# Kernel tuning notes

Measured on AMD Instinct MI355X. Metric: run time of the kernel, lower is better.

The kernel has to match this reference:

```python
import jax, jax.numpy as jnp
import numpy as np

N_NODES = 50000


def gcn_conv(x, edge_index, W, b, n_nodes):
    # Linear transform first (as in PyG GCNConv), then normalized aggregation
    xw = x @ W  # [N, out]
    src, dst = edge_index[0], edge_index[1]
    loops = jnp.arange(n_nodes, dtype=src.dtype)
    s = jnp.concatenate([src, loops])  # add self-loops
    d = jnp.concatenate([dst, loops])
    deg = jax.ops.segment_sum(jnp.ones_like(s, dtype=xw.dtype), d, num_segments=n_nodes)
    dinv = jnp.where(deg > 0, jax.lax.rsqrt(deg), 0.0)
    norm = dinv[s] * dinv[d]  # [E+N]
    msg = xw[s] * norm[:, None]  # gather + scale
    out = jax.ops.segment_sum(msg, d, num_segments=n_nodes)  # scatter-add
    return out + b


def setup_inputs() -> dict:
    key = jax.random.key(0)
    k1, k2, k3, k4 = jax.random.split(key, 4)
    in_dim, hidden = 128, 128
    n_edges = 625000
    x = jax.random.normal(k1, (N_NODES, in_dim), dtype=jnp.float32)
    edge_index = jax.random.randint(k2, (2, n_edges), 0, N_NODES, dtype=jnp.int64)
    # glorot-ish scale
    W1 = jax.random.normal(k3, (in_dim, hidden), dtype=jnp.float32) * (1.0 / np.sqrt(in_dim))
    b1 = jnp.zeros((hidden,), dtype=jnp.float32)
    W2 = jax.random.normal(k4, (hidden, hidden), dtype=jnp.float32) * (1.0 / np.sqrt(hidden))
    b2 = jnp.zeros((hidden,), dtype=jnp.float32)
    return {"x": x, "edge_index": edge_index, "W1": W1, "b1": b1, "W2": W2, "b2": b2}


def reference(x, edge_index, W1, b1, W2, b2):
    n = x.shape[0]
    h = gcn_conv(x, edge_index, W1, b1, n)
    h = jax.nn.relu(h)
    # dropout(p=0.3) is identity in eval mode
    h = gcn_conv(h, edge_index, W2, b2, n)
    return jax.nn.relu(h)
```

## Files before the change

kernel.cpp:

```cpp
#include <hip/hip_runtime.h>
#include <hip/hip_bf16.h>

#define NNODES 50000
#define BKT 64
#define LP 136
#define NC 25
#define CCAP 40960
#define P0EPT 16
#define FINE 128
#define AGG_BLOCKS 2048

typedef short bf16x8 __attribute__((ext_vector_type(8)));
typedef float f32x4 __attribute__((ext_vector_type(4)));

__device__ __forceinline__ unsigned short f2bf_rn(float f) {
    unsigned int u = __float_as_uint(f);
    return (unsigned short)((u + 0x7fffu + ((u >> 16) & 1u)) >> 16);
}
__device__ __forceinline__ float bf_lo(unsigned int u) { return __uint_as_float(u << 16); }
__device__ __forceinline__ float bf_hi(unsigned int u) { return __uint_as_float(u & 0xffff0000u); }


__global__ __launch_bounds__(256) void k_wt(const float* __restrict__ W1,
                                            const float* __restrict__ W2,
                                            unsigned short* __restrict__ WT1,
                                            unsigned short* __restrict__ WT2,
                                            int* __restrict__ gcnt) {
    __shared__ float tile[128 * 129];
    int b = blockIdx.x, t = threadIdx.x;
    if (b == 0 && t < NC) gcnt[t] = 0;
    const float* W = b ? W2 : W1;
    unsigned short* WT = b ? WT2 : WT1;
    for (int idx = t; idx < 128 * 128; idx += 256)
        tile[(idx >> 7) * 129 + (idx & 127)] = W[idx];
    __syncthreads();
    for (int idx = t; idx < 128 * 128; idx += 256) {
        int c = idx >> 7, k = idx & 127;
        WT[c * 128 + k] = f2bf_rn(tile[k * 129 + c]);
    }
}


__global__ __launch_bounds__(256) void k_part(const int* __restrict__ src,
                                              const int* __restrict__ dst,
                                              int* __restrict__ gcnt,
                                              unsigned int* __restrict__ rec, int E) {
    __shared__ int lhist[NC];
    __shared__ int lbase[NC];
    int t = threadIdx.x;
    if (t < NC) lhist[t] = 0;
    __syncthreads();

    int e0 = (blockIdx.x * 256 + t) * P0EPT;
    unsigned int r[P0EPT];
    int cc[P0EPT];
    int lofs[P0EPT];
    int nv = 0;
    if (e0 + P0EPT <= E) {
#pragma unroll
        for (int k4 = 0; k4 < P0EPT / 4; ++k4) {
            int4 s4 = *(const int4*)&src[e0 + k4 * 4];
            int4 d4 = *(const int4*)&dst[e0 + k4 * 4];
            int ss[4] = {s4.x, s4.y, s4.z, s4.w};
            int dd[4] = {d4.x, d4.y, d4.z, d4.w};
#pragma unroll
            for (int k = 0; k < 4; ++k) {
                r[k4 * 4 + k] = (unsigned)(ss[k] & 0xffff) | ((unsigned)dd[k] << 16);
                cc[k4 * 4 + k] = dd[k] >> 11;
            }
        }
        nv = P0EPT;
    } else {
#pragma unroll
        for (int k = 0; k < P0EPT; ++k) {
            int e = e0 + k;
            if (e < E) {
                int s = src[e], d = dst[e];
                r[k] = (unsigned)(s & 0xffff) | ((unsigned)d << 16);
                cc[k] = d >> 11;
                nv = k + 1;
            } else {
                cc[k] = 0;
            }
        }
    }
#pragma unroll
    for (int k = 0; k < P0EPT; ++k)
        if (k < nv) lofs[k] = atomicAdd(&lhist[cc[k]], 1);
    __syncthreads();
    if (t < NC) lbase[t] = atomicAdd(&gcnt[t], lhist[t]);
    __syncthreads();
#pragma unroll
    for (int k = 0; k < P0EPT; ++k)
        if (k < nv) {
            int pos = lbase[cc[k]] + lofs[k];
            if (pos < CCAP) rec[(size_t)cc[k] * CCAP + pos] = r[k];
        }
}


__global__ __launch_bounds__(256) void k_bucket2(const unsigned int* __restrict__ rec,
                                                 const int* __restrict__ gcnt,
                                                 int* __restrict__ cnt,
                                                 unsigned short* __restrict__ bkt, int N) {
    __shared__ unsigned short lbkt[FINE * BKT];
    __shared__ int lcnt[FINE];
    int t = threadIdx.x, b = blockIdx.x;
    int lo = b * FINE;
    int c = lo >> 11;
    for (int i = t; i < FINE; i += 256) lcnt[i] = 0;
    __syncthreads();

    int M = min(gcnt[c], CCAP);
    const unsigned int* R = &rec[(size_t)c * CCAP];
    auto process = [&](unsigned int rv) {
        unsigned dl = (rv >> 16) - (unsigned)lo;
        if (dl < (unsigned)FINE) {
            int p = atomicAdd(&lcnt[dl], 1);
            if (p < BKT) lbkt[dl * BKT + p] = (unsigned short)(rv & 0xffffu);
        }
    };
    int M4 = M >> 2;
    for (int i = t; i < M4; i += 256) {
        uint4 q = *(const uint4*)&R[i * 4];
        process(q.x); process(q.y); process(q.z); process(q.w);
    }
    for (int i = (M4 << 2) + t; i < M; i += 256) process(R[i]);
    __syncthreads();

    if (t < FINE && lo + t < N) cnt[lo + t] = lcnt[t];
    for (int i = t; i < FINE * 8; i += 256) {
        int node = i >> 3;
        if (lo + node < N)
            ((uint4*)&bkt[(size_t)lo * BKT])[i] = ((const uint4*)lbkt)[i];
    }
}


__device__ __forceinline__ void gather_wsum(const unsigned int* __restrict__ xwb,
                                            const float* __restrict__ dinv,
                                            const unsigned short* __restrict__ bp,
                                            int degc, int lane,
                                            float& ax, float& ay) {
    float px = 0.f, py = 0.f;
    int j = 0;
    for (; j + 8 <= degc; j += 8) {
        int4 q = *(const int4*)&bp[j];
        int s0 = q.x & 0xffff, s1 = (int)((unsigned)q.x >> 16);
        int s2 = q.y & 0xffff, s3 = (int)((unsigned)q.y >> 16);
        int s4 = q.z & 0xffff, s5 = (int)((unsigned)q.z >> 16);
        int s6 = q.w & 0xffff, s7 = (int)((unsigned)q.w >> 16);
        unsigned int u0 = xwb[(size_t)s0 * 64 + lane];
        unsigned int u1 = xwb[(size_t)s1 * 64 + lane];
        unsigned int u2 = xwb[(size_t)s2 * 64 + lane];
        unsigned int u3 = xwb[(size_t)s3 * 64 + lane];
        unsigned int u4 = xwb[(size_t)s4 * 64 + lane];
        unsigned int u5 = xwb[(size_t)s5 * 64 + lane];
        unsigned int u6 = xwb[(size_t)s6 * 64 + lane];
        unsigned int u7 = xwb[(size_t)s7 * 64 + lane];
        float w0 = dinv[s0], w1 = dinv[s1], w2 = dinv[s2], w3 = dinv[s3];
        float w4 = dinv[s4], w5 = dinv[s5], w6 = dinv[s6], w7 = dinv[s7];
        ax = fmaf(bf_lo(u0), w0, ax);  ay = fmaf(bf_hi(u0), w0, ay);
        px = fmaf(bf_lo(u1), w1, px);  py = fmaf(bf_hi(u1), w1, py);
        ax = fmaf(bf_lo(u2), w2, ax);  ay = fmaf(bf_hi(u2), w2, ay);
        px = fmaf(bf_lo(u3), w3, px);  py = fmaf(bf_hi(u3), w3, py);
        ax = fmaf(bf_lo(u4), w4, ax);  ay = fmaf(bf_hi(u4), w4, ay);
        px = fmaf(bf_lo(u5), w5, px);  py = fmaf(bf_hi(u5), w5, py);
        ax = fmaf(bf_lo(u6), w6, ax);  ay = fmaf(bf_hi(u6), w6, ay);
        px = fmaf(bf_lo(u7), w7, px);  py = fmaf(bf_hi(u7), w7, py);
    }
    if (j + 4 <= degc) {
        int2 q = *(const int2*)&bp[j];
        int s0 = q.x & 0xffff, s1 = (int)((unsigned)q.x >> 16);
        int s2 = q.y & 0xffff, s3 = (int)((unsigned)q.y >> 16);
        unsigned int u0 = xwb[(size_t)s0 * 64 + lane];
        unsigned int u1 = xwb[(size_t)s1 * 64 + lane];
        unsigned int u2 = xwb[(size_t)s2 * 64 + lane];
        unsigned int u3 = xwb[(size_t)s3 * 64 + lane];
        float w0 = dinv[s0], w1 = dinv[s1], w2 = dinv[s2], w3 = dinv[s3];
        ax = fmaf(bf_lo(u0), w0, ax);  ay = fmaf(bf_hi(u0), w0, ay);
        px = fmaf(bf_lo(u1), w1, px);  py = fmaf(bf_hi(u1), w1, py);
        ax = fmaf(bf_lo(u2), w2, ax);  ay = fmaf(bf_hi(u2), w2, ay);
        px = fmaf(bf_lo(u3), w3, px);  py = fmaf(bf_hi(u3), w3, py);
        j += 4;
    }
    for (; j < degc; ++j) {
        int s = bp[j];
        float wv = dinv[s];
        unsigned int u = xwb[(size_t)s * 64 + lane];
        ax = fmaf(bf_lo(u), wv, ax);
        ay = fmaf(bf_hi(u), wv, ay);
    }
    ax += px;
    ay += py;
}


__device__ __forceinline__ void gather_sum(const unsigned int* __restrict__ xwb,
                                           const unsigned short* __restrict__ bp,
                                           int degc, int lane,
                                           float& ax, float& ay) {
    float px = 0.f, py = 0.f;
    int j = 0;
    for (; j + 8 <= degc; j += 8) {
        int4 q = *(const int4*)&bp[j];
        int s0 = q.x & 0xffff, s1 = (int)((unsigned)q.x >> 16);
        int s2 = q.y & 0xffff, s3 = (int)((unsigned)q.y >> 16);
        int s4 = q.z & 0xffff, s5 = (int)((unsigned)q.z >> 16);
        int s6 = q.w & 0xffff, s7 = (int)((unsigned)q.w >> 16);
        unsigned int u0 = xwb[(size_t)s0 * 64 + lane];
        unsigned int u1 = xwb[(size_t)s1 * 64 + lane];
        unsigned int u2 = xwb[(size_t)s2 * 64 + lane];
        unsigned int u3 = xwb[(size_t)s3 * 64 + lane];
        unsigned int u4 = xwb[(size_t)s4 * 64 + lane];
        unsigned int u5 = xwb[(size_t)s5 * 64 + lane];
        unsigned int u6 = xwb[(size_t)s6 * 64 + lane];
        unsigned int u7 = xwb[(size_t)s7 * 64 + lane];
        ax += bf_lo(u0);  ay += bf_hi(u0);
        px += bf_lo(u1);  py += bf_hi(u1);
        ax += bf_lo(u2);  ay += bf_hi(u2);
        px += bf_lo(u3);  py += bf_hi(u3);
        ax += bf_lo(u4);  ay += bf_hi(u4);
        px += bf_lo(u5);  py += bf_hi(u5);
        ax += bf_lo(u6);  ay += bf_hi(u6);
        px += bf_lo(u7);  py += bf_hi(u7);
    }
    if (j + 4 <= degc) {
        int2 q = *(const int2*)&bp[j];
        int s0 = q.x & 0xffff, s1 = (int)((unsigned)q.x >> 16);
        int s2 = q.y & 0xffff, s3 = (int)((unsigned)q.y >> 16);
        unsigned int u0 = xwb[(size_t)s0 * 64 + lane];
        unsigned int u1 = xwb[(size_t)s1 * 64 + lane];
        unsigned int u2 = xwb[(size_t)s2 * 64 + lane];
        unsigned int u3 = xwb[(size_t)s3 * 64 + lane];
        ax += bf_lo(u0);  ay += bf_hi(u0);
        px += bf_lo(u1);  py += bf_hi(u1);
        ax += bf_lo(u2);  ay += bf_hi(u2);
        px += bf_lo(u3);  py += bf_hi(u3);
        j += 4;
    }
    for (; j < degc; ++j) {
        int s = bp[j];
        unsigned int u = xwb[(size_t)s * 64 + lane];
        ax += bf_lo(u);
        ay += bf_hi(u);
    }
    ax += px;
    ay += py;
}


__global__ __launch_bounds__(256) void k_gemm1(const float* __restrict__ X,
                                               const unsigned short* __restrict__ WT,
                                               unsigned short* __restrict__ Yb, int n) {
    __shared__ unsigned short Ep[64 * LP];
    int t = threadIdx.x;
    int lane = t & 63, w = t >> 6;
    int m = lane & 15, quad = lane >> 4;
    int base = blockIdx.x * 64 + w * 16;
    int row = min(base + m, n - 1);

    bf16x8 a[4];
#pragma unroll
    for (int kt = 0; kt < 4; ++kt) {
        const float* pa = &X[(size_t)row * 128 + kt * 32 + quad * 8];
        float4 v0 = *(const float4*)pa;
        float4 v1 = *(const float4*)(pa + 4);
        a[kt][0] = (short)f2bf_rn(v0.x); a[kt][1] = (short)f2bf_rn(v0.y);
        a[kt][2] = (short)f2bf_rn(v0.z); a[kt][3] = (short)f2bf_rn(v0.w);
        a[kt][4] = (short)f2bf_rn(v1.x); a[kt][5] = (short)f2bf_rn(v1.y);
        a[kt][6] = (short)f2bf_rn(v1.z); a[kt][7] = (short)f2bf_rn(v1.w);
    }

    f32x4 acc[8];
#pragma unroll
    for (int i = 0; i < 8; ++i) acc[i] = f32x4{0.f, 0.f, 0.f, 0.f};
#pragma unroll
    for (int kt = 0; kt < 4; ++kt) {
        int ko = kt * 32 + quad * 8;
#pragma unroll
        for (int ct = 0; ct < 8; ++ct) {
            bf16x8 bfrag = *(const bf16x8*)&WT[(ct * 16 + m) * 128 + ko];
            acc[ct] = __builtin_amdgcn_mfma_f32_16x16x32_bf16(a[kt], bfrag, acc[ct], 0, 0, 0);
        }
    }

    unsigned short* ep = &Ep[w * 16 * LP];
#pragma unroll
    for (int ct = 0; ct < 8; ++ct)
#pragma unroll
        for (int r = 0; r < 4; ++r)
            ep[(quad * 4 + r) * LP + ct * 16 + m] = f2bf_rn(acc[ct][r]);
    __syncthreads();
    int rr = lane & 15, cc = lane >> 4;
    int orow = base + rr;
    if (orow < n) {
#pragma unroll
        for (int i2 = 0; i2 < 4; ++i2)
            ((uint4*)&Yb[(size_t)orow * 128])[cc * 4 + i2] =
                *(const uint4*)&ep[rr * LP + (cc * 4 + i2) * 8];
    }
}


__global__ __launch_bounds__(256) void k_dinv(const int* __restrict__ cnt,
                                              float* __restrict__ dinv, int N) {
    int i = blockIdx.x * 256 + threadIdx.x;
    if (i < N) dinv[i] = rsqrtf((float)cnt[i] + 1.0f);
}


__global__ __launch_bounds__(1024, 8) void k_aggemm(const unsigned int* __restrict__ xw1,
                                                    const int* __restrict__ cnt,
                                                    const unsigned short* __restrict__ bkt,
                                                    const float* __restrict__ dinv,
                                                    const float* __restrict__ bias,
                                                    const unsigned short* __restrict__ WT2,
                                                    unsigned short* __restrict__ xw2, int n) {
    __shared__ unsigned short Wl[128 * LP];
    __shared__ unsigned short At[64 * LP];
    __shared__ float dsw[64];
    int t = threadIdx.x, lane = t & 63, w = t >> 6;
    int m = lane & 15, quad = lane >> 4;
    int base = blockIdx.x * 64;

    for (int idx = t; idx < 128 * 16; idx += 1024) {
        int r = idx >> 4, c8 = (idx & 15) << 3;
        *(uint4*)&Wl[r * LP + c8] = *(const uint4*)&WT2[r * 128 + c8];
    }
    float bx = bias[lane * 2], by = bias[lane * 2 + 1];

#pragma unroll
    for (int k = 0; k < 4; ++k) {
        int nd = w * 4 + k;
        int i = min(base + nd, n - 1);
        int degc = min(cnt[i], BKT);
        float di = dinv[i];
        unsigned int v0 = xw1[(size_t)i * 64 + lane];
        float ax = di * bf_lo(v0), ay = di * bf_hi(v0);
        gather_wsum(xw1, dinv, &bkt[(size_t)i * BKT], degc, lane, ax, ay);
        ax = fmaxf(fmaf(di, ax, bx), 0.0f);
        ay = fmaxf(fmaf(di, ay, by), 0.0f);
        ((unsigned int*)&At[nd * LP])[lane] =
            (unsigned)f2bf_rn(ax) | ((unsigned)f2bf_rn(ay) << 16);
        if (lane == 0) dsw[nd] = di;
    }
    __syncthreads();

    int ct = w & 7, rb = w >> 3;
    f32x4 acc0 = f32x4{0.f, 0.f, 0.f, 0.f};
    f32x4 acc1 = f32x4{0.f, 0.f, 0.f, 0.f};
#pragma unroll
    for (int kt = 0; kt < 4; ++kt) {
        int ko = kt * 32 + quad * 8;
        bf16x8 bfrag = *(const bf16x8*)&Wl[(ct * 16 + m) * LP + ko];
        bf16x8 a0 = *(const bf16x8*)&At[(rb * 16 + m) * LP + ko];
        bf16x8 a1 = *(const bf16x8*)&At[((rb + 2) * 16 + m) * LP + ko];
        acc0 = __builtin_amdgcn_mfma_f32_16x16x32_bf16(a0, bfrag, acc0, 0, 0, 0);
        acc1 = __builtin_amdgcn_mfma_f32_16x16x32_bf16(a1, bfrag, acc1, 0, 0, 0);
    }
    __syncthreads();

#pragma unroll
    for (int r = 0; r < 4; ++r) {
        int r0 = rb * 16 + quad * 4 + r;
        int r1 = (rb + 2) * 16 + quad * 4 + r;
        At[r0 * LP + ct * 16 + m] = f2bf_rn(acc0[r] * dsw[r0]);
        At[r1 * LP + ct * 16 + m] = f2bf_rn(acc1[r] * dsw[r1]);
    }
    __syncthreads();

    int row = t >> 4, q = t & 15;
    int orow = base + row;
    if (orow < n)
        *(uint4*)&xw2[(size_t)orow * 128 + q * 8] = *(const uint4*)&At[row * LP + q * 8];
}


__global__ __launch_bounds__(256) void k_agg(const unsigned int* __restrict__ xwb,
                                             const int* __restrict__ cnt,
                                             const unsigned short* __restrict__ bkt,
                                             const float* __restrict__ dinv,
                                             const float* __restrict__ bias,
                                             float* __restrict__ out, int n) {
    int lane = threadIdx.x & 63;
    int gw = (blockIdx.x * 256 + threadIdx.x) >> 6;
    int nw = (gridDim.x * 256) >> 6;
    float bx = bias[lane * 2], by = bias[lane * 2 + 1];
    for (int i = gw; i < n; i += nw) {
        int degc = min(cnt[i], BKT);
        float di = dinv[i];
        unsigned int v0 = xwb[(size_t)i * 64 + lane];
        float ax = bf_lo(v0), ay = bf_hi(v0);
        gather_sum(xwb, &bkt[(size_t)i * BKT], degc, lane, ax, ay);
        ax = fmaxf(fmaf(di, ax, bx), 0.0f);
        ay = fmaxf(fmaf(di, ay, by), 0.0f);
        ((float2*)out)[(size_t)i * 64 + lane] = make_float2(ax, ay);
    }
}


extern "C" void kernel_launch(void* const* d_in, const int* in_sizes, int n_in,
                              void* d_out, int out_size, void* d_ws, size_t ws_size,
                              hipStream_t stream) {
    const float* x  = (const float*)d_in[0];
    const int*   ei = (const int*)d_in[1];
    const float* W1 = (const float*)d_in[2];
    const float* b1 = (const float*)d_in[3];
    const float* W2 = (const float*)d_in[4];
    const float* b2 = (const float*)d_in[5];
    float* out = (float*)d_out;

    const int N = NNODES;
    const int E = in_sizes[1] / 2;
    const int* src = ei;
    const int* dst = ei + E;

    char* p = (char*)d_ws;
    size_t off = 0;
    auto take = [&](size_t bytes) -> void* {
        void* r = p + off;
        off = (off + bytes + 255) & ~(size_t)255;
        return r;
    };
    int* cnt = (int*)take((size_t)N * 4);
    unsigned short* bkt = (unsigned short*)take((size_t)N * BKT * 2);
    unsigned short* w1t = (unsigned short*)take(128 * 128 * 2);
    unsigned short* w2t = (unsigned short*)take(128 * 128 * 2);
    unsigned short* xw1 = (unsigned short*)take((size_t)N * 128 * 2);
    unsigned short* xw2 = (unsigned short*)take((size_t)N * 128 * 2);
    float* dinv = (float*)take((size_t)N * 4);
    int* gcnt = (int*)take(NC * 4);
    unsigned int* rec = (unsigned int*)take((size_t)NC * CCAP * 4);

    const int NB = (N + 255) / 256;
    const int P0B = (E + 256 * P0EPT - 1) / (256 * P0EPT);
    const int P1B = (N + FINE - 1) / FINE;
    const int GB = (N + 63) / 64;

    k_wt<<<2, 256, 0, stream>>>(W1, W2, w1t, w2t, gcnt);
    k_part<<<P0B, 256, 0, stream>>>(src, dst, gcnt, rec, E);
    k_gemm1<<<GB, 256, 0, stream>>>(x, w1t, xw1, N);
    k_bucket2<<<P1B, 256, 0, stream>>>(rec, gcnt, cnt, bkt, N);
    k_dinv<<<NB, 256, 0, stream>>>(cnt, dinv, N);
    k_aggemm<<<GB, 1024, 0, stream>>>((const unsigned int*)xw1, cnt, bkt, dinv,
                                      b1, w2t, xw2, N);
    k_agg<<<AGG_BLOCKS, 256, 0, stream>>>((const unsigned int*)xw2, cnt, bkt, dinv,
                                          b2, out, N);
}
```

Measured before the change: 195.8 us.

## Merge prep, bucket, dinv and first GEMM kernels into fewer launches

Folds the weight transpose and edge partitioning into one kernel, with the first two blocks doing the transposes, and zeroes the chunk counters with a memset instead. The fine bucketing, the dinv computation and the first GEMM now share a single launch, split by block index. FINE is doubled to 256, so each bucket block covers more nodes and the partitioned record chunks are rescanned half as often. The cost is that partition blocks now reserve the large transpose tile in LDS, which can lower their occupancy. The merged kernel also carries more branch code.

```diff
diff --git a/kernel.cpp b/kernel.cpp
--- a/kernel.cpp
+++ b/kernel.cpp
@@ -7,7 +7,7 @@
 #define NC 25
 #define CCAP 40960
 #define P0EPT 16
-#define FINE 128
+#define FINE 256
 #define AGG_BLOCKS 2048
 
 typedef short bf16x8 __attribute__((ext_vector_type(8)));
@@ -21,37 +21,34 @@
 __device__ __forceinline__ float bf_hi(unsigned int u) { return __uint_as_float(u & 0xffff0000u); }
 
 
-__global__ __launch_bounds__(256) void k_wt(const float* __restrict__ W1,
-                                            const float* __restrict__ W2,
-                                            unsigned short* __restrict__ WT1,
-                                            unsigned short* __restrict__ WT2,
-                                            int* __restrict__ gcnt) {
-    __shared__ float tile[128 * 129];
-    int b = blockIdx.x, t = threadIdx.x;
-    if (b == 0 && t < NC) gcnt[t] = 0;
-    const float* W = b ? W2 : W1;
-    unsigned short* WT = b ? WT2 : WT1;
-    for (int idx = t; idx < 128 * 128; idx += 256)
-        tile[(idx >> 7) * 129 + (idx & 127)] = W[idx];
-    __syncthreads();
-    for (int idx = t; idx < 128 * 128; idx += 256) {
-        int c = idx >> 7, k = idx & 127;
-        WT[c * 128 + k] = f2bf_rn(tile[k * 129 + c]);
-    }
-}
-
-
-__global__ __launch_bounds__(256) void k_part(const int* __restrict__ src,
+__global__ __launch_bounds__(256) void k_prep(const float* __restrict__ W1,
+                                              const float* __restrict__ W2,
+                                              unsigned short* __restrict__ WT1,
+                                              unsigned short* __restrict__ WT2,
+                                              const int* __restrict__ src,
                                               const int* __restrict__ dst,
                                               int* __restrict__ gcnt,
                                               unsigned int* __restrict__ rec, int E) {
-    __shared__ int lhist[NC];
-    __shared__ int lbase[NC];
-    int t = threadIdx.x;
+    __shared__ float tile[128 * 129];
+    int b = blockIdx.x, t = threadIdx.x;
+    if (b < 2) {
+        const float* W = b ? W2 : W1;
+        unsigned short* WT = b ? WT2 : WT1;
+        for (int idx = t; idx < 128 * 128; idx += 256)
+            tile[(idx >> 7) * 129 + (idx & 127)] = W[idx];
+        __syncthreads();
+        for (int idx = t; idx < 128 * 128; idx += 256) {
+            int c = idx >> 7, k = idx & 127;
+            WT[c * 128 + k] = f2bf_rn(tile[k * 129 + c]);
+        }
+        return;
+    }
+    int* lhist = (int*)tile;
+    int* lbase = lhist + NC;
     if (t < NC) lhist[t] = 0;
     __syncthreads();
 
-    int e0 = (blockIdx.x * 256 + t) * P0EPT;
+    int e0 = ((b - 2) * 256 + t) * P0EPT;
     unsigned int r[P0EPT];
     int cc[P0EPT];
     int lofs[P0EPT];
@@ -99,40 +96,100 @@
 }
 
 
-__global__ __launch_bounds__(256) void k_bucket2(const unsigned int* __restrict__ rec,
-                                                 const int* __restrict__ gcnt,
-                                                 int* __restrict__ cnt,
-                                                 unsigned short* __restrict__ bkt, int N) {
-    __shared__ unsigned short lbkt[FINE * BKT];
-    __shared__ int lcnt[FINE];
+__global__ __launch_bounds__(256) void k_build(const unsigned int* __restrict__ rec,
+                                               const int* __restrict__ gcnt,
+                                               int* __restrict__ cnt,
+                                               unsigned short* __restrict__ bkt,
+                                               float* __restrict__ dinv,
+                                               const float* __restrict__ X,
+                                               const unsigned short* __restrict__ WT,
+                                               unsigned short* __restrict__ Yb,
+                                               int n, int P1B) {
+    __shared__ __align__(16) unsigned char smem[FINE * BKT * 2 + FINE * 4];
     int t = threadIdx.x, b = blockIdx.x;
-    int lo = b * FINE;
-    int c = lo >> 11;
-    for (int i = t; i < FINE; i += 256) lcnt[i] = 0;
-    __syncthreads();
-
-    int M = min(gcnt[c], CCAP);
-    const unsigned int* R = &rec[(size_t)c * CCAP];
-    auto process = [&](unsigned int rv) {
-        unsigned dl = (rv >> 16) - (unsigned)lo;
-        if (dl < (unsigned)FINE) {
-            int p = atomicAdd(&lcnt[dl], 1);
-            if (p < BKT) lbkt[dl * BKT + p] = (unsigned short)(rv & 0xffffu);
-        }
-    };
-    int M4 = M >> 2;
-    for (int i = t; i < M4; i += 256) {
-        uint4 q = *(const uint4*)&R[i * 4];
-        process(q.x); process(q.y); process(q.z); process(q.w);
-    }
-    for (int i = (M4 << 2) + t; i < M; i += 256) process(R[i]);
-    __syncthreads();
-
-    if (t < FINE && lo + t < N) cnt[lo + t] = lcnt[t];
-    for (int i = t; i < FINE * 8; i += 256) {
-        int node = i >> 3;
-        if (lo + node < N)
-            ((uint4*)&bkt[(size_t)lo * BKT])[i] = ((const uint4*)lbkt)[i];
+    if (b < P1B) {
+        unsigned short* lbkt = (unsigned short*)smem;
+        int* lcnt = (int*)(smem + FINE * BKT * 2);
+        int lo = b * FINE;
+        int c = lo >> 11;
+        for (int i = t; i < FINE; i += 256) lcnt[i] = 0;
+        __syncthreads();
+
+        int M = min(gcnt[c], CCAP);
+        const unsigned int* R = &rec[(size_t)c * CCAP];
+        auto process = [&](unsigned int rv) {
+            unsigned dl = (rv >> 16) - (unsigned)lo;
+            if (dl < (unsigned)FINE) {
+                int p = atomicAdd(&lcnt[dl], 1);
+                if (p < BKT) lbkt[dl * BKT + p] = (unsigned short)(rv & 0xffffu);
+            }
+        };
+        int M4 = M >> 2;
+        for (int i = t; i < M4; i += 256) {
+            uint4 q = *(const uint4*)&R[i * 4];
+            process(q.x); process(q.y); process(q.z); process(q.w);
+        }
+        for (int i = (M4 << 2) + t; i < M; i += 256) process(R[i]);
+        __syncthreads();
+
+        if (lo + t < n) {
+            int cv = lcnt[t];
+            cnt[lo + t] = cv;
+            dinv[lo + t] = rsqrtf((float)cv + 1.0f);
+        }
+        for (int i = t; i < FINE * 8; i += 256) {
+            int node = i >> 3;
+            if (lo + node < n)
+                ((uint4*)&bkt[(size_t)lo * BKT])[i] = ((const uint4*)lbkt)[i];
+        }
+        return;
+    }
+    unsigned short* Ep = (unsigned short*)smem;
+    int gb = b - P1B;
+    int lane = t & 63, w = t >> 6;
+    int m = lane & 15, quad = lane >> 4;
+    int base = gb * 64 + w * 16;
+    int row = min(base + m, n - 1);
+
+    bf16x8 a[4];
+#pragma unroll
+    for (int kt = 0; kt < 4; ++kt) {
+        const float* pa = &X[(size_t)row * 128 + kt * 32 + quad * 8];
+        float4 v0 = *(const float4*)pa;
+        float4 v1 = *(const float4*)(pa + 4);
+        a[kt][0] = (short)f2bf_rn(v0.x); a[kt][1] = (short)f2bf_rn(v0.y);
+        a[kt][2] = (short)f2bf_rn(v0.z); a[kt][3] = (short)f2bf_rn(v0.w);
+        a[kt][4] = (short)f2bf_rn(v1.x); a[kt][5] = (short)f2bf_rn(v1.y);
+        a[kt][6] = (short)f2bf_rn(v1.z); a[kt][7] = (short)f2bf_rn(v1.w);
+    }
+
+    f32x4 acc[8];
+#pragma unroll
+    for (int i = 0; i < 8; ++i) acc[i] = f32x4{0.f, 0.f, 0.f, 0.f};
+#pragma unroll
+    for (int kt = 0; kt < 4; ++kt) {
+        int ko = kt * 32 + quad * 8;
+#pragma unroll
+        for (int ct = 0; ct < 8; ++ct) {
+            bf16x8 bfrag = *(const bf16x8*)&WT[(ct * 16 + m) * 128 + ko];
+            acc[ct] = __builtin_amdgcn_mfma_f32_16x16x32_bf16(a[kt], bfrag, acc[ct], 0, 0, 0);
+        }
+    }
+
+    unsigned short* ep = &Ep[w * 16 * LP];
+#pragma unroll
+    for (int ct = 0; ct < 8; ++ct)
+#pragma unroll
+        for (int r = 0; r < 4; ++r)
+            ep[(quad * 4 + r) * LP + ct * 16 + m] = f2bf_rn(acc[ct][r]);
+    __syncthreads();
+    int rr = lane & 15, cc2 = lane >> 4;
+    int orow = base + rr;
+    if (orow < n) {
+#pragma unroll
+        for (int i2 = 0; i2 < 4; ++i2)
+            ((uint4*)&Yb[(size_t)orow * 128])[cc2 * 4 + i2] =
+                *(const uint4*)&ep[rr * LP + (cc2 * 4 + i2) * 8];
     }
 }
 
@@ -250,66 +307,6 @@
 }
 
 
-__global__ __launch_bounds__(256) void k_gemm1(const float* __restrict__ X,
-                                               const unsigned short* __restrict__ WT,
-                                               unsigned short* __restrict__ Yb, int n) {
-    __shared__ unsigned short Ep[64 * LP];
-    int t = threadIdx.x;
-    int lane = t & 63, w = t >> 6;
-    int m = lane & 15, quad = lane >> 4;
-    int base = blockIdx.x * 64 + w * 16;
-    int row = min(base + m, n - 1);
-
-    bf16x8 a[4];
-#pragma unroll
-    for (int kt = 0; kt < 4; ++kt) {
-        const float* pa = &X[(size_t)row * 128 + kt * 32 + quad * 8];
-        float4 v0 = *(const float4*)pa;
-        float4 v1 = *(const float4*)(pa + 4);
-        a[kt][0] = (short)f2bf_rn(v0.x); a[kt][1] = (short)f2bf_rn(v0.y);
-        a[kt][2] = (short)f2bf_rn(v0.z); a[kt][3] = (short)f2bf_rn(v0.w);
-        a[kt][4] = (short)f2bf_rn(v1.x); a[kt][5] = (short)f2bf_rn(v1.y);
-        a[kt][6] = (short)f2bf_rn(v1.z); a[kt][7] = (short)f2bf_rn(v1.w);
-    }
-
-    f32x4 acc[8];
-#pragma unroll
-    for (int i = 0; i < 8; ++i) acc[i] = f32x4{0.f, 0.f, 0.f, 0.f};
-#pragma unroll
-    for (int kt = 0; kt < 4; ++kt) {
-        int ko = kt * 32 + quad * 8;
-#pragma unroll
-        for (int ct = 0; ct < 8; ++ct) {
-            bf16x8 bfrag = *(const bf16x8*)&WT[(ct * 16 + m) * 128 + ko];
-            acc[ct] = __builtin_amdgcn_mfma_f32_16x16x32_bf16(a[kt], bfrag, acc[ct], 0, 0, 0);
-        }
-    }
-
-    unsigned short* ep = &Ep[w * 16 * LP];
-#pragma unroll
-    for (int ct = 0; ct < 8; ++ct)
-#pragma unroll
-        for (int r = 0; r < 4; ++r)
-            ep[(quad * 4 + r) * LP + ct * 16 + m] = f2bf_rn(acc[ct][r]);
-    __syncthreads();
-    int rr = lane & 15, cc = lane >> 4;
-    int orow = base + rr;
-    if (orow < n) {
-#pragma unroll
-        for (int i2 = 0; i2 < 4; ++i2)
-            ((uint4*)&Yb[(size_t)orow * 128])[cc * 4 + i2] =
-                *(const uint4*)&ep[rr * LP + (cc * 4 + i2) * 8];
-    }
-}
-
-
-__global__ __launch_bounds__(256) void k_dinv(const int* __restrict__ cnt,
-                                              float* __restrict__ dinv, int N) {
-    int i = blockIdx.x * 256 + threadIdx.x;
-    if (i < N) dinv[i] = rsqrtf((float)cnt[i] + 1.0f);
-}
-
-
 __global__ __launch_bounds__(1024, 8) void k_aggemm(const unsigned int* __restrict__ xw1,
                                                     const int* __restrict__ cnt,
                                                     const unsigned short* __restrict__ bkt,
@@ -433,16 +430,13 @@
     int* gcnt = (int*)take(NC * 4);
     unsigned int* rec = (unsigned int*)take((size_t)NC * CCAP * 4);
 
-    const int NB = (N + 255) / 256;
     const int P0B = (E + 256 * P0EPT - 1) / (256 * P0EPT);
     const int P1B = (N + FINE - 1) / FINE;
     const int GB = (N + 63) / 64;
 
-    k_wt<<<2, 256, 0, stream>>>(W1, W2, w1t, w2t, gcnt);
-    k_part<<<P0B, 256, 0, stream>>>(src, dst, gcnt, rec, E);
-    k_gemm1<<<GB, 256, 0, stream>>>(x, w1t, xw1, N);
-    k_bucket2<<<P1B, 256, 0, stream>>>(rec, gcnt, cnt, bkt, N);
-    k_dinv<<<NB, 256, 0, stream>>>(cnt, dinv, N);
+    hipMemsetAsync(gcnt, 0, NC * sizeof(int), stream);
+    k_prep<<<2 + P0B, 256, 0, stream>>>(W1, W2, w1t, w2t, src, dst, gcnt, rec, E);
+    k_build<<<P1B + GB, 256, 0, stream>>>(rec, gcnt, cnt, bkt, dinv, x, w1t, xw1, N, P1B);
     k_aggemm<<<GB, 1024, 0, stream>>>((const unsigned int*)xw1, cnt, bkt, dinv,
                                       b1, w2t, xw2, N);
     k_agg<<<AGG_BLOCKS, 256, 0, stream>>>((const unsigned int*)xw2, cnt, bkt, dinv,
```

Measured after the change: 179.7 us. 8.2% less time.
